# Kernel optimization log

Hardware: AMD Instinct MI355X
Metric: run time of the kernel (lower is better)

## Reference

```python
import jax, jax.numpy as jnp
import numpy as np

N_NODES = 50000


def _gine_conv(x, src, dst, edge_attr, ew, eb, w1, b1, w2, b2, eps=0.0):
    # message: ReLU(x_j + Linear(edge_attr))  -- PyG GINEConv with edge_dim lin
    m = jax.nn.relu(x[src] + edge_attr @ ew + eb)          # [E, D]
    agg = jax.ops.segment_sum(m, dst, num_segments=N_NODES)  # [N, D]
    h = (1.0 + eps) * x + agg
    # nn: Linear -> ReLU -> Linear
    return jax.nn.relu(h @ w1 + b1) @ w2 + b2


def setup_inputs() -> dict:
    key = jax.random.key(0)
    ks = jax.random.split(key, 16)
    Cin, H, Cout, Ed = 128, 256, 256, 16
    E = 800000
    x = jax.random.normal(ks[0], (N_NODES, Cin), dtype=jnp.float32)
    edge_index = jax.random.randint(ks[1], (2, E), 0, N_NODES, dtype=jnp.int32)
    edge_attr = jax.random.normal(ks[2], (E, Ed), dtype=jnp.float32)

    def lin(k, fan_in, fan_out):
        s = 1.0 / np.sqrt(fan_in)
        kw, kb = jax.random.split(k)
        w = jax.random.uniform(kw, (fan_in, fan_out), minval=-s, maxval=s, dtype=jnp.float32)
        b = jax.random.uniform(kb, (fan_out,), minval=-s, maxval=s, dtype=jnp.float32)
        return w, b

    e1_w, e1_b = lin(ks[3], Ed, Cin)     # conv1 edge lin: edge_dim -> in_channels
    l11_w, l11_b = lin(ks[4], Cin, H)    # conv1 MLP layer 1
    l12_w, l12_b = lin(ks[5], H, Cout)   # conv1 MLP layer 2
    e2_w, e2_b = lin(ks[6], Ed, H)       # conv2 edge lin: edge_dim -> hidden
    l21_w, l21_b = lin(ks[7], H, H)      # conv2 MLP layer 1
    l22_w, l22_b = lin(ks[8], H, Cout)   # conv2 MLP layer 2
    return {
        "x": x, "edge_index": edge_index, "edge_attr": edge_attr,
        "e1_w": e1_w, "e1_b": e1_b, "l11_w": l11_w, "l11_b": l11_b,
        "l12_w": l12_w, "l12_b": l12_b,
        "e2_w": e2_w, "e2_b": e2_b, "l21_w": l21_w, "l21_b": l21_b,
        "l22_w": l22_w, "l22_b": l22_b,
    }


def reference(x, edge_index, edge_attr,
              e1_w, e1_b, l11_w, l11_b, l12_w, l12_b,
              e2_w, e2_b, l21_w, l21_b, l22_w, l22_b):
    src, dst = edge_index[0], edge_index[1]
    h = _gine_conv(x, src, dst, edge_attr, e1_w, e1_b, l11_w, l11_b, l12_w, l12_b)
    h = _gine_conv(h, src, dst, edge_attr, e2_w, e2_b, l21_w, l21_b, l22_w, l22_b)
    return h
```

## Files before the change

kernel.cpp:

```cpp
#include <hip/hip_runtime.h>
#include <type_traits>

#define N_NODES 50000

using short8  = __attribute__((ext_vector_type(8))) short;
using floatx4 = __attribute__((ext_vector_type(4))) float;
using f32x2   = __attribute__((ext_vector_type(2))) float;

__device__ inline unsigned short f2b(float f) {
    unsigned u = __float_as_uint(f);
    u += 0x7FFFu + ((u >> 16) & 1u);
    return (unsigned short)(u >> 16);
}
__device__ inline float b2f(unsigned short h) {
    return __uint_as_float(((unsigned)h) << 16);
}

__device__ inline f32x2 pk_fma_lo(f32x2 a, f32x2 b, f32x2 c) {
    f32x2 d;
    asm("v_pk_fma_f32 %0, %1, %2, %3 op_sel_hi:[0,1,1]"
        : "=v"(d) : "v"(a), "v"(b), "v"(c));
    return d;
}
__device__ inline f32x2 pk_fma_hi(f32x2 a, f32x2 b, f32x2 c) {
    f32x2 d;
    asm("v_pk_fma_f32 %0, %1, %2, %3 op_sel:[1,0,0] op_sel_hi:[1,1,1]"
        : "=v"(d) : "v"(a), "v"(b), "v"(c));
    return d;
}
__device__ inline f32x2 pk_add(f32x2 a, f32x2 b) {
    f32x2 d;
    asm("v_pk_add_f32 %0, %1, %2" : "=v"(d) : "v"(a), "v"(b));
    return d;
}

__global__ __launch_bounds__(256) void zero_int_kernel(int* __restrict__ p, int n)
{
    int i = blockIdx.x * 256 + threadIdx.x;
    if (i < n) p[i] = 0;
}

__global__ __launch_bounds__(256) void hist_kernel(const int* __restrict__ dstv,
                                                   int* __restrict__ cnt, int E)
{
    int e = blockIdx.x * 256 + threadIdx.x;
    if (e < E) atomicAdd(&cnt[dstv[e]], 1);
}

__global__ __launch_bounds__(256) void scanA_kernel(const int* __restrict__ cnt,
                                                    int* __restrict__ row_start,
                                                    int* __restrict__ bsum, int n)
{
    __shared__ int s[256];
    int t = threadIdx.x;
    int i = blockIdx.x * 256 + t;
    int val = (i < n) ? cnt[i] : 0;
    s[t] = val;
    __syncthreads();
#pragma unroll
    for (int off = 1; off < 256; off <<= 1) {
        int v = (t >= off) ? s[t - off] : 0;
        __syncthreads();
        s[t] += v;
        __syncthreads();
    }
    if (i < n) row_start[i] = s[t] - val;
    if (t == 255) bsum[blockIdx.x] = s[255];
}

__global__ __launch_bounds__(256) void scanB_kernel(int* __restrict__ bsum, int nb)
{
    __shared__ int s[256];
    int t = threadIdx.x;
    int val = (t < nb) ? bsum[t] : 0;
    s[t] = val;
    __syncthreads();
#pragma unroll
    for (int off = 1; off < 256; off <<= 1) {
        int v = (t >= off) ? s[t - off] : 0;
        __syncthreads();
        s[t] += v;
        __syncthreads();
    }
    if (t < nb) bsum[t] = s[t] - val;
}

__global__ __launch_bounds__(256) void scanC_kernel(int* __restrict__ row_start,
                                                    int* __restrict__ woff,
                                                    const int* __restrict__ bsum, int n)
{
    int i = blockIdx.x * 256 + threadIdx.x;
    if (i < n) {
        int v = row_start[i] + bsum[blockIdx.x];
        row_start[i] = v;
        woff[i] = v;
    }
}

__global__ __launch_bounds__(256) void scatter_kernel(const int* __restrict__ srcv,
                                                      const int* __restrict__ dstv,
                                                      int* __restrict__ woff,
                                                      int2* __restrict__ sorted2, int E)
{
    int e = blockIdx.x * 256 + threadIdx.x;
    if (e < E) {
        int pos = atomicAdd(&woff[dstv[e]], 1);
        sorted2[pos] = make_int2(srcv[e], e);
    }
}

__global__ __launch_bounds__(256) void castT_kernel(const float* __restrict__ w,
                                                    unsigned short* __restrict__ out, int K)
{
    int i = blockIdx.x * 256 + threadIdx.x;
    if (i < K * 256) {
        int k = i >> 8, c = i & 255;
        out[c * K + k] = f2b(w[i]);
    }
}

template<int D, bool XB>
__global__ __launch_bounds__(256) void agg_kernel(
    const float*          __restrict__ xf,
    const unsigned short* __restrict__ xb,
    const float*          __restrict__ ea,
    const float*          __restrict__ ew,
    const float*          __restrict__ ebias,
    const int*            __restrict__ row_start,
    const int*            __restrict__ cnt,
    const int2*           __restrict__ sorted2,
    float*                __restrict__ agg,
    int N)
{
    constexpr int DPL = D / 64;
    constexpr int NP  = DPL / 2;
    using XT = std::conditional_t<XB, ushort4,
               std::conditional_t<DPL == 2, float2, float4>>;

    const int lane = threadIdx.x & 63;
    const int node = blockIdx.x * 4 + (threadIdx.x >> 6);
    if (node >= N) return;
    const int d0 = lane * DPL;

    f32x2 wrp[16 * NP];
#pragma unroll
    for (int k = 0; k < 16; ++k) {
        if constexpr (NP == 1) {
            float2 w2 = *reinterpret_cast<const float2*>(ew + k * D + d0);
            wrp[k] = f32x2{w2.x, w2.y};
        } else {
            float4 w4 = *reinterpret_cast<const float4*>(ew + k * D + d0);
            wrp[k * 2 + 0] = f32x2{w4.x, w4.y};
            wrp[k * 2 + 1] = f32x2{w4.z, w4.w};
        }
    }
    f32x2 bx[NP];
#pragma unroll
    for (int p = 0; p < NP; ++p)
        bx[p] = f32x2{ebias[d0 + p * 2], ebias[d0 + p * 2 + 1]};

    f32x2 acc[NP];
#pragma unroll
    for (int p = 0; p < NP; ++p) acc[p] = f32x2{0.f, 0.f};

    const int s0 = __builtin_amdgcn_readfirstlane(row_start[node]);
    const int c  = __builtin_amdgcn_readfirstlane(cnt[node]);

    for (int base = 0; base < c; base += 64) {
        const int cc = min(64, c - base);

        int2 pr = make_int2(0, 0);
        if (lane < cc) pr = sorted2[s0 + base + lane];

        float4 eA0, eA1, eA2, eA3; XT xA;
        float4 eB0, eB1, eB2, eB3; XT xB;

        auto LOADA = [&](int idx) {
            int s = __builtin_amdgcn_readlane(pr.x, idx);
            int e = __builtin_amdgcn_readlane(pr.y, idx);
            const float4* p = reinterpret_cast<const float4*>(ea + (size_t)e * 16);
            eA0 = p[0]; eA1 = p[1]; eA2 = p[2]; eA3 = p[3];
            if constexpr (XB) xA = *reinterpret_cast<const XT*>(xb + (size_t)s * D + d0);
            else              xA = *reinterpret_cast<const XT*>(xf + (size_t)s * D + d0);
        };
        auto LOADB = [&](int idx) {
            int s = __builtin_amdgcn_readlane(pr.x, idx);
            int e = __builtin_amdgcn_readlane(pr.y, idx);
            const float4* p = reinterpret_cast<const float4*>(ea + (size_t)e * 16);
            eB0 = p[0]; eB1 = p[1]; eB2 = p[2]; eB3 = p[3];
            if constexpr (XB) xB = *reinterpret_cast<const XT*>(xb + (size_t)s * D + d0);
            else              xB = *reinterpret_cast<const XT*>(xf + (size_t)s * D + d0);
        };

        auto COMPUTE = [&](const float4& E0, const float4& E1,
                           const float4& E2, const float4& E3, const XT& X) {
            f32x2 ap[8] = {f32x2{E0.x, E0.y}, f32x2{E0.z, E0.w},
                           f32x2{E1.x, E1.y}, f32x2{E1.z, E1.w},
                           f32x2{E2.x, E2.y}, f32x2{E2.z, E2.w},
                           f32x2{E3.x, E3.y}, f32x2{E3.z, E3.w}};
            f32x2 m[NP];
            if constexpr (XB) {
                m[0] = pk_add(bx[0], f32x2{b2f(X.x), b2f(X.y)});
                m[1] = pk_add(bx[1], f32x2{b2f(X.z), b2f(X.w)});
            } else if constexpr (NP == 1) {
                m[0] = pk_add(bx[0], f32x2{X.x, X.y});
            } else {
                m[0] = pk_add(bx[0], f32x2{X.x, X.y});
                m[1] = pk_add(bx[1], f32x2{X.z, X.w});
            }
#pragma unroll
            for (int kp = 0; kp < 8; ++kp) {
#pragma unroll
                for (int p = 0; p < NP; ++p)
                    m[p] = pk_fma_lo(ap[kp], wrp[(2 * kp) * NP + p], m[p]);
#pragma unroll
                for (int p = 0; p < NP; ++p)
                    m[p] = pk_fma_hi(ap[kp], wrp[(2 * kp + 1) * NP + p], m[p]);
            }
#pragma unroll
            for (int p = 0; p < NP; ++p) {
                f32x2 r{fmaxf(m[p].x, 0.f), fmaxf(m[p].y, 0.f)};
                acc[p] = pk_add(acc[p], r);
            }
        };

        LOADA(0);
        int i = 0;
        while (true) {
            if (i + 1 < cc) LOADB(i + 1);
            COMPUTE(eA0, eA1, eA2, eA3, xA);
            ++i; if (i >= cc) break;
            if (i + 1 < cc) LOADA(i + 1);
            COMPUTE(eB0, eB1, eB2, eB3, xB);
            ++i; if (i >= cc) break;
        }
    }

    if constexpr (NP == 1)
        *reinterpret_cast<float2*>(agg + (size_t)node * D + d0) =
            make_float2(acc[0].x, acc[0].y);
    else
        *reinterpret_cast<float4*>(agg + (size_t)node * D + d0) =
            make_float4(acc[0].x, acc[0].y, acc[1].x, acc[1].y);
}

template<int DIN, bool L1>
__global__ __launch_bounds__(256) void node_mfma_kernel(
    const float*          __restrict__ basef,
    const unsigned short* __restrict__ baseb,
    const float*          __restrict__ agg,
    const unsigned short* __restrict__ w1T,
    const float*          __restrict__ b1,
    const unsigned short* __restrict__ w2T,
    const float*          __restrict__ b2,
    unsigned short*       __restrict__ outb,
    float*                __restrict__ outf,
    int N)
{
    __shared__ unsigned short hs[64 * DIN];
    __shared__ unsigned short ts[64 * 256];
    const int tid = threadIdx.x;
    const int n0 = blockIdx.x * 64;

#pragma unroll
    for (int it = 0; it < (64 * DIN) / (256 * 8); ++it) {
        int flat = (it * 256 + tid) * 8;
        int r = flat / DIN, c = flat % DIN;
        int node = n0 + r;
        float v[8];
        if (node < N) {
            const float* ap = agg + (size_t)node * DIN + c;
            float4 a0 = *reinterpret_cast<const float4*>(ap);
            float4 a1 = *reinterpret_cast<const float4*>(ap + 4);
            float a[8] = {a0.x, a0.y, a0.z, a0.w, a1.x, a1.y, a1.z, a1.w};
            if constexpr (L1) {
                const float* bp = basef + (size_t)node * DIN + c;
                float4 x0 = *reinterpret_cast<const float4*>(bp);
                float4 x1 = *reinterpret_cast<const float4*>(bp + 4);
                float xx[8] = {x0.x, x0.y, x0.z, x0.w, x1.x, x1.y, x1.z, x1.w};
#pragma unroll
                for (int j = 0; j < 8; ++j) v[j] = a[j] + xx[j];
            } else {
                short8 xv = *reinterpret_cast<const short8*>(baseb + (size_t)node * DIN + c);
#pragma unroll
                for (int j = 0; j < 8; ++j) v[j] = a[j] + b2f((unsigned short)xv[j]);
            }
        } else {
#pragma unroll
            for (int j = 0; j < 8; ++j) v[j] = 0.f;
        }
        short8 o;
#pragma unroll
        for (int j = 0; j < 8; ++j) o[j] = (short)f2b(v[j]);
        *reinterpret_cast<short8*>(&hs[r * DIN + (c ^ ((r & 7) << 3))]) = o;
    }
    __syncthreads();

    const int wv = tid >> 6, lane = tid & 63;
    const int lr = lane & 15, lk = (lane >> 4) * 8;
    const int colbase = wv * 64;

    floatx4 acc[4][4];
#pragma unroll
    for (int n = 0; n < 4; ++n) {
        float bn = b1[colbase + n * 16 + lr];
#pragma unroll
        for (int m = 0; m < 4; ++m) acc[m][n] = floatx4{bn, bn, bn, bn};
    }
#pragma unroll
    for (int kk = 0; kk < DIN; kk += 32) {
        short8 af[4], bf[4];
#pragma unroll
        for (int m = 0; m < 4; ++m) {
            int row = m * 16 + lr;
            af[m] = *reinterpret_cast<const short8*>(
                &hs[row * DIN + ((kk + lk) ^ ((row & 7) << 3))]);
        }
#pragma unroll
        for (int n = 0; n < 4; ++n) {
            int col = colbase + n * 16 + lr;
            bf[n] = *reinterpret_cast<const short8*>(w1T + (size_t)col * DIN + kk + lk);
        }
#pragma unroll
        for (int m = 0; m < 4; ++m)
#pragma unroll
            for (int n = 0; n < 4; ++n)
                acc[m][n] = __builtin_amdgcn_mfma_f32_16x16x32_bf16(af[m], bf[n], acc[m][n], 0, 0, 0);
    }
#pragma unroll
    for (int m = 0; m < 4; ++m)
#pragma unroll
        for (int n = 0; n < 4; ++n)
#pragma unroll
            for (int r = 0; r < 4; ++r) {
                int row = m * 16 + (lane >> 4) * 4 + r;
                int col = colbase + n * 16 + lr;
                ts[row * 256 + (col ^ ((row & 7) << 3))] = f2b(fmaxf(acc[m][n][r], 0.f));
            }
    __syncthreads();

    floatx4 acc2[4][4];
#pragma unroll
    for (int n = 0; n < 4; ++n) {
        float bn = b2[colbase + n * 16 + lr];
#pragma unroll
        for (int m = 0; m < 4; ++m) acc2[m][n] = floatx4{bn, bn, bn, bn};
    }
#pragma unroll
    for (int kk = 0; kk < 256; kk += 32) {
        short8 af[4], bf[4];
#pragma unroll
        for (int m = 0; m < 4; ++m) {
            int row = m * 16 + lr;
            af[m] = *reinterpret_cast<const short8*>(
                &ts[row * 256 + ((kk + lk) ^ ((row & 7) << 3))]);
        }
#pragma unroll
        for (int n = 0; n < 4; ++n) {
            int col = colbase + n * 16 + lr;
            bf[n] = *reinterpret_cast<const short8*>(w2T + (size_t)col * 256 + kk + lk);
        }
#pragma unroll
        for (int m = 0; m < 4; ++m)
#pragma unroll
            for (int n = 0; n < 4; ++n)
                acc2[m][n] = __builtin_amdgcn_mfma_f32_16x16x32_bf16(af[m], bf[n], acc2[m][n], 0, 0, 0);
    }
#pragma unroll
    for (int m = 0; m < 4; ++m)
#pragma unroll
        for (int n = 0; n < 4; ++n)
#pragma unroll
            for (int r = 0; r < 4; ++r) {
                int row = m * 16 + (lane >> 4) * 4 + r;
                int node = n0 + row;
                int col = colbase + n * 16 + lr;
                if (node < N) {
                    if constexpr (L1) outb[(size_t)node * 256 + col] = f2b(acc2[m][n][r]);
                    else              outf[(size_t)node * 256 + col] = acc2[m][n][r];
                }
            }
}

extern "C" void kernel_launch(void* const* d_in, const int* in_sizes, int n_in,
                              void* d_out, int out_size, void* d_ws, size_t ws_size,
                              hipStream_t stream)
{
    const float* x    = (const float*)d_in[0];
    const int*   ei   = (const int*)  d_in[1];
    const float* ea   = (const float*)d_in[2];
    const float* e1w  = (const float*)d_in[3];
    const float* e1b  = (const float*)d_in[4];
    const float* w11  = (const float*)d_in[5];
    const float* b11  = (const float*)d_in[6];
    const float* w12  = (const float*)d_in[7];
    const float* b12  = (const float*)d_in[8];
    const float* e2w  = (const float*)d_in[9];
    const float* e2b  = (const float*)d_in[10];
    const float* w21  = (const float*)d_in[11];
    const float* b21  = (const float*)d_in[12];
    const float* w22  = (const float*)d_in[13];
    const float* b22  = (const float*)d_in[14];

    const int E = in_sizes[1] / 2;
    const int N = N_NODES;
    const int* src = ei;
    const int* dst = ei + E;

    char* cur = (char*)d_ws;
    float* aggb = (float*)cur;            cur += (size_t)N * 256 * 4;
    int*   cnt       = (int*)cur;         cur += (size_t)N * 4;
    int*   row_start = (int*)cur;         cur += (size_t)N * 4;
    int*   woff      = (int*)cur;         cur += (size_t)N * 4;
    int*   bsum      = (int*)cur;         cur += 256 * 4;
    int2*  sorted2   = (int2*)cur;        cur += (size_t)E * 8;
    unsigned short* h1b  = (unsigned short*)cur; cur += (size_t)N * 256 * 2;
    unsigned short* w11T = (unsigned short*)cur; cur += 128 * 256 * 2;
    unsigned short* w12T = (unsigned short*)cur; cur += 256 * 256 * 2;
    unsigned short* w21T = (unsigned short*)cur; cur += 256 * 256 * 2;
    unsigned short* w22T = (unsigned short*)cur; cur += 256 * 256 * 2;
    float* outp = (float*)d_out;

    const int nbN = (N + 255) / 256;
    const int nbE = (E + 255) / 256;

    castT_kernel<<<(128 * 256 + 255) / 256, 256, 0, stream>>>(w11, w11T, 128);
    castT_kernel<<<256, 256, 0, stream>>>(w12, w12T, 256);
    castT_kernel<<<256, 256, 0, stream>>>(w21, w21T, 256);
    castT_kernel<<<256, 256, 0, stream>>>(w22, w22T, 256);

    zero_int_kernel<<<nbN, 256, 0, stream>>>(cnt, N);
    hist_kernel<<<nbE, 256, 0, stream>>>(dst, cnt, E);
    scanA_kernel<<<nbN, 256, 0, stream>>>(cnt, row_start, bsum, N);
    scanB_kernel<<<1, 256, 0, stream>>>(bsum, nbN);
    scanC_kernel<<<nbN, 256, 0, stream>>>(row_start, woff, bsum, N);
    scatter_kernel<<<nbE, 256, 0, stream>>>(src, dst, woff, sorted2, E);

    const int nbAgg  = (N + 3) / 4;
    const int nbNode = (N + 63) / 64;

    agg_kernel<128, false><<<nbAgg, 256, 0, stream>>>(
        x, nullptr, ea, e1w, e1b, row_start, cnt, sorted2, aggb, N);
    node_mfma_kernel<128, true><<<nbNode, 256, 0, stream>>>(
        x, nullptr, aggb, w11T, b11, w12T, b12, h1b, nullptr, N);

    agg_kernel<256, true><<<nbAgg, 256, 0, stream>>>(
        nullptr, h1b, ea, e2w, e2b, row_start, cnt, sorted2, aggb, N);
    node_mfma_kernel<256, false><<<nbNode, 256, 0, stream>>>(
        nullptr, h1b, aggb, w21T, b21, w22T, b22, nullptr, outp, N);
}
```

Baseline: 439.8 us.

## Persistent agg kernel staging edge attrs into LDS with async double buffering

Makes the aggregation kernel persistent: each wave walks over nodes with a grid stride. For each node it stages the edge-attribute rows into a per-wave double-buffered LDS area using global_load_lds, and it prefetches the next node's CSR metadata and edge list while computing the current node. Inside the inner loop, edge attributes are now read from LDS instead of through scalar-indexed global loads. The grid size is fixed and occupancy hints are added to launch_bounds. The cost is explicit vmcnt(0) waits, which may serialize the staging, and the fixed grid sizes may underfill or imbalance the GPU.

Result: slower. 476.3 us (+8.3%).

```diff
diff --git a/kernel.cpp b/kernel.cpp
--- a/kernel.cpp
+++ b/kernel.cpp
@@ -120,7 +120,7 @@
 }
 
 template<int D, bool XB>
-__global__ __launch_bounds__(256) void agg_kernel(
+__global__ __launch_bounds__(256, (D == 256) ? 3 : 4) void agg_kernel(
     const float*          __restrict__ xf,
     const unsigned short* __restrict__ xb,
     const float*          __restrict__ ea,
@@ -137,10 +137,14 @@
     using XT = std::conditional_t<XB, ushort4,
                std::conditional_t<DPL == 2, float2, float4>>;
 
+    __shared__ float sEA[4][2][64][16];
+
     const int lane = threadIdx.x & 63;
-    const int node = blockIdx.x * 4 + (threadIdx.x >> 6);
+    const int w    = threadIdx.x >> 6;
+    const int W    = gridDim.x * 4;
+    int node = blockIdx.x * 4 + w;
+    const int d0 = lane * DPL;
     if (node >= N) return;
-    const int d0 = lane * DPL;
 
     f32x2 wrp[16 * NP];
 #pragma unroll
@@ -157,91 +161,140 @@
     f32x2 bx[NP];
 #pragma unroll
     for (int p = 0; p < NP; ++p)
-        bx[p] = f32x2{ebias[d0 + p * 2], ebias[d0 + p * 2 + 1]};
+        bx[p] = f32x2{ebias[d0 + 2 * p], ebias[d0 + 2 * p + 1]};
 
     f32x2 acc[NP];
-#pragma unroll
-    for (int p = 0; p < NP; ++p) acc[p] = f32x2{0.f, 0.f};
-
-    const int s0 = __builtin_amdgcn_readfirstlane(row_start[node]);
-    const int c  = __builtin_amdgcn_readfirstlane(cnt[node]);
-
-    for (int base = 0; base < c; base += 64) {
-        const int cc = min(64, c - base);
-
-        int2 pr = make_int2(0, 0);
-        if (lane < cc) pr = sorted2[s0 + base + lane];
-
-        float4 eA0, eA1, eA2, eA3; XT xA;
-        float4 eB0, eB1, eB2, eB3; XT xB;
-
-        auto LOADA = [&](int idx) {
-            int s = __builtin_amdgcn_readlane(pr.x, idx);
-            int e = __builtin_amdgcn_readlane(pr.y, idx);
-            const float4* p = reinterpret_cast<const float4*>(ea + (size_t)e * 16);
-            eA0 = p[0]; eA1 = p[1]; eA2 = p[2]; eA3 = p[3];
+
+    auto STAGE = [&](int2 prv, int cb, int bi) {
+        const int sweeps = (cb + 15) >> 4;
+        const int chunk  = lane & 3;
+        const int sl0    = lane >> 2;
+        for (int j = 0; j < sweeps; ++j) {
+            int sl  = j * 16 + sl0;
+            int eid = __shfl(prv.y, sl);
+            if (sl >= cb) eid = 0;
+            const float* gp = ea + (size_t)eid * 16 + chunk * 4;
+            __builtin_amdgcn_global_load_lds(gp, &sEA[w][bi][j * 16][0], 16, 0, 0);
+        }
+    };
+
+    auto COMPUTE = [&](const float4& E0, const float4& E1,
+                       const float4& E2, const float4& E3, const XT& X) {
+        f32x2 ap[8] = {f32x2{E0.x, E0.y}, f32x2{E0.z, E0.w},
+                       f32x2{E1.x, E1.y}, f32x2{E1.z, E1.w},
+                       f32x2{E2.x, E2.y}, f32x2{E2.z, E2.w},
+                       f32x2{E3.x, E3.y}, f32x2{E3.z, E3.w}};
+        f32x2 m[NP];
+        if constexpr (XB) {
+            m[0] = pk_add(bx[0], f32x2{b2f(X.x), b2f(X.y)});
+            m[1] = pk_add(bx[1], f32x2{b2f(X.z), b2f(X.w)});
+        } else if constexpr (NP == 1) {
+            m[0] = pk_add(bx[0], f32x2{X.x, X.y});
+        } else {
+            m[0] = pk_add(bx[0], f32x2{X.x, X.y});
+            m[1] = pk_add(bx[1], f32x2{X.z, X.w});
+        }
+#pragma unroll
+        for (int kp = 0; kp < 8; ++kp) {
+#pragma unroll
+            for (int p = 0; p < NP; ++p)
+                m[p] = pk_fma_lo(ap[kp], wrp[(2 * kp) * NP + p], m[p]);
+#pragma unroll
+            for (int p = 0; p < NP; ++p)
+                m[p] = pk_fma_hi(ap[kp], wrp[(2 * kp + 1) * NP + p], m[p]);
+        }
+#pragma unroll
+        for (int p = 0; p < NP; ++p) {
+            f32x2 r{fmaxf(m[p].x, 0.f), fmaxf(m[p].y, 0.f)};
+            acc[p] = pk_add(acc[p], r);
+        }
+    };
+
+    auto RUN = [&](int cb, int bi, int2 prv) {
+        if (cb <= 0) return;
+        float4 EA0, EA1, EA2, EA3, EB0, EB1, EB2, EB3;
+        XT xA, xB;
+        auto LA = [&](int i) {
+            const float4* rp = reinterpret_cast<const float4*>(&sEA[w][bi][i][0]);
+            EA0 = rp[0]; EA1 = rp[1]; EA2 = rp[2]; EA3 = rp[3];
+            int s = __builtin_amdgcn_readlane(prv.x, i);
             if constexpr (XB) xA = *reinterpret_cast<const XT*>(xb + (size_t)s * D + d0);
             else              xA = *reinterpret_cast<const XT*>(xf + (size_t)s * D + d0);
         };
-        auto LOADB = [&](int idx) {
-            int s = __builtin_amdgcn_readlane(pr.x, idx);
-            int e = __builtin_amdgcn_readlane(pr.y, idx);
-            const float4* p = reinterpret_cast<const float4*>(ea + (size_t)e * 16);
-            eB0 = p[0]; eB1 = p[1]; eB2 = p[2]; eB3 = p[3];
+        auto LB = [&](int i) {
+            const float4* rp = reinterpret_cast<const float4*>(&sEA[w][bi][i][0]);
+            EB0 = rp[0]; EB1 = rp[1]; EB2 = rp[2]; EB3 = rp[3];
+            int s = __builtin_amdgcn_readlane(prv.x, i);
             if constexpr (XB) xB = *reinterpret_cast<const XT*>(xb + (size_t)s * D + d0);
             else              xB = *reinterpret_cast<const XT*>(xf + (size_t)s * D + d0);
         };
-
-        auto COMPUTE = [&](const float4& E0, const float4& E1,
-                           const float4& E2, const float4& E3, const XT& X) {
-            f32x2 ap[8] = {f32x2{E0.x, E0.y}, f32x2{E0.z, E0.w},
-                           f32x2{E1.x, E1.y}, f32x2{E1.z, E1.w},
-                           f32x2{E2.x, E2.y}, f32x2{E2.z, E2.w},
-                           f32x2{E3.x, E3.y}, f32x2{E3.z, E3.w}};
-            f32x2 m[NP];
-            if constexpr (XB) {
-                m[0] = pk_add(bx[0], f32x2{b2f(X.x), b2f(X.y)});
-                m[1] = pk_add(bx[1], f32x2{b2f(X.z), b2f(X.w)});
-            } else if constexpr (NP == 1) {
-                m[0] = pk_add(bx[0], f32x2{X.x, X.y});
-            } else {
-                m[0] = pk_add(bx[0], f32x2{X.x, X.y});
-                m[1] = pk_add(bx[1], f32x2{X.z, X.w});
-            }
-#pragma unroll
-            for (int kp = 0; kp < 8; ++kp) {
-#pragma unroll
-                for (int p = 0; p < NP; ++p)
-                    m[p] = pk_fma_lo(ap[kp], wrp[(2 * kp) * NP + p], m[p]);
-#pragma unroll
-                for (int p = 0; p < NP; ++p)
-                    m[p] = pk_fma_hi(ap[kp], wrp[(2 * kp + 1) * NP + p], m[p]);
-            }
-#pragma unroll
-            for (int p = 0; p < NP; ++p) {
-                f32x2 r{fmaxf(m[p].x, 0.f), fmaxf(m[p].y, 0.f)};
-                acc[p] = pk_add(acc[p], r);
-            }
-        };
-
-        LOADA(0);
+        LA(0);
         int i = 0;
         while (true) {
-            if (i + 1 < cc) LOADB(i + 1);
-            COMPUTE(eA0, eA1, eA2, eA3, xA);
-            ++i; if (i >= cc) break;
-            if (i + 1 < cc) LOADA(i + 1);
-            COMPUTE(eB0, eB1, eB2, eB3, xB);
-            ++i; if (i >= cc) break;
-        }
-    }
-
-    if constexpr (NP == 1)
-        *reinterpret_cast<float2*>(agg + (size_t)node * D + d0) =
-            make_float2(acc[0].x, acc[0].y);
-    else
-        *reinterpret_cast<float4*>(agg + (size_t)node * D + d0) =
-            make_float4(acc[0].x, acc[0].y, acc[1].x, acc[1].y);
+            if (i + 1 < cb) LB(i + 1);
+            COMPUTE(EA0, EA1, EA2, EA3, xA);
+            ++i; if (i >= cb) break;
+            if (i + 1 < cb) LA(i + 1);
+            COMPUTE(EB0, EB1, EB2, EB3, xB);
+            ++i; if (i >= cb) break;
+        }
+    };
+
+    int s0 = __builtin_amdgcn_readfirstlane(row_start[node]);
+    int c  = __builtin_amdgcn_readfirstlane(cnt[node]);
+    int cb = min(c, 64);
+    int2 pr = make_int2(0, 0);
+    if (lane < cb) pr = sorted2[s0 + lane];
+    STAGE(pr, cb, 0);
+    int buf = 0;
+
+    int nnode = node + W;
+    int ns0 = 0, nc = 0;
+    if (nnode < N) { ns0 = row_start[nnode]; nc = cnt[nnode]; }
+
+    asm volatile("s_waitcnt vmcnt(0)" ::: "memory");
+
+    while (true) {
+        int  ncb = 0;
+        int2 npr = make_int2(0, 0);
+        if (nnode < N) {
+            ns0 = __builtin_amdgcn_readfirstlane(ns0);
+            nc  = __builtin_amdgcn_readfirstlane(nc);
+            ncb = min(nc, 64);
+            if (lane < ncb) npr = sorted2[ns0 + lane];
+        }
+        int nnnode = nnode + W;
+        int nns0 = 0, nnc = 0;
+        if (nnnode < N) { nns0 = row_start[nnnode]; nnc = cnt[nnnode]; }
+
+#pragma unroll
+        for (int p = 0; p < NP; ++p) acc[p] = f32x2{0.f, 0.f};
+
+        RUN(cb, buf, pr);
+
+        for (int base = 64; base < c; base += 64) {
+            int cb2 = min(64, c - base);
+            int2 pv = make_int2(0, 0);
+            if (lane < cb2) pv = sorted2[s0 + base + lane];
+            STAGE(pv, cb2, buf);
+            asm volatile("s_waitcnt vmcnt(0)" ::: "memory");
+            RUN(cb2, buf, pv);
+        }
+
+        if constexpr (NP == 1)
+            *reinterpret_cast<float2*>(agg + (size_t)node * D + d0) =
+                make_float2(acc[0].x, acc[0].y);
+        else
+            *reinterpret_cast<float4*>(agg + (size_t)node * D + d0) =
+                make_float4(acc[0].x, acc[0].y, acc[1].x, acc[1].y);
+
+        if (nnode >= N) break;
+        STAGE(npr, ncb, buf ^ 1);
+        asm volatile("s_waitcnt vmcnt(0)" ::: "memory");
+
+        node = nnode; s0 = ns0; c = nc; cb = ncb; pr = npr; buf ^= 1;
+        nnode = nnnode; ns0 = nns0; nc = nnc;
+    }
 }
 
 template<int DIN, bool L1>
@@ -436,15 +489,14 @@
     scanC_kernel<<<nbN, 256, 0, stream>>>(row_start, woff, bsum, N);
     scatter_kernel<<<nbE, 256, 0, stream>>>(src, dst, woff, sorted2, E);
 
-    const int nbAgg  = (N + 3) / 4;
     const int nbNode = (N + 63) / 64;
 
-    agg_kernel<128, false><<<nbAgg, 256, 0, stream>>>(
+    agg_kernel<128, false><<<1024, 256, 0, stream>>>(
         x, nullptr, ea, e1w, e1b, row_start, cnt, sorted2, aggb, N);
     node_mfma_kernel<128, true><<<nbNode, 256, 0, stream>>>(
         x, nullptr, aggb, w11T, b11, w12T, b12, h1b, nullptr, N);
 
-    agg_kernel<256, true><<<nbAgg, 256, 0, stream>>>(
+    agg_kernel<256, true><<<768, 256, 0, stream>>>(
         nullptr, h1b, ea, e2w, e2b, row_start, cnt, sorted2, aggb, N);
     node_mfma_kernel<256, false><<<nbNode, 256, 0, stream>>>(
         nullptr, h1b, aggb, w21T, b21, w22T, b22, nullptr, outp, N);
```

## Stage edge-linear weights in LDS and process edges in pairs

Applied to the files above, without the earlier changes.

The aggregation kernel now loads the 16xD edge-linear weights and bias into shared memory once per block and reads them from LDS inside the inner loop, instead of holding them in registers. This frees a large register array, which should allow more waves per CU. The edge loop also changes from a software-pipelined A/B prefetch to processing two edges per iteration so each LDS weight read serves both. The cost is extra LDS traffic on every iteration and the loss of the explicit prefetch overlap between load and compute.

Result: faster. 415.4 us (-5.5%).

```diff
diff --git a/kernel.cpp b/kernel.cpp
--- a/kernel.cpp
+++ b/kernel.cpp
@@ -28,10 +28,8 @@
         : "=v"(d) : "v"(a), "v"(b), "v"(c));
     return d;
 }
-__device__ inline f32x2 pk_add(f32x2 a, f32x2 b) {
-    f32x2 d;
-    asm("v_pk_add_f32 %0, %1, %2" : "=v"(d) : "v"(a), "v"(b));
-    return d;
+__device__ inline f32x2 vrelu(f32x2 a) {
+    return __builtin_elementwise_max(a, f32x2{0.f, 0.f});
 }
 
 __global__ __launch_bounds__(256) void zero_int_kernel(int* __restrict__ p, int n)
@@ -137,27 +135,33 @@
     using XT = std::conditional_t<XB, ushort4,
                std::conditional_t<DPL == 2, float2, float4>>;
 
-    const int lane = threadIdx.x & 63;
-    const int node = blockIdx.x * 4 + (threadIdx.x >> 6);
+    __shared__ float wlds[17 * D];
+
+    const int tid = threadIdx.x;
+#pragma unroll
+    for (int ci = tid; ci < (17 * D) / 4; ci += 256) {
+        int f0 = ci * 4;
+        float4 v;
+        if (f0 < 16 * D) v = *reinterpret_cast<const float4*>(ew + f0);
+        else             v = *reinterpret_cast<const float4*>(ebias + (f0 - 16 * D));
+        *reinterpret_cast<float4*>(&wlds[f0]) = v;
+    }
+    __syncthreads();
+
+    const int lane = tid & 63;
+    const int node = blockIdx.x * 4 + (tid >> 6);
     if (node >= N) return;
     const int d0 = lane * DPL;
 
-    f32x2 wrp[16 * NP];
-#pragma unroll
-    for (int k = 0; k < 16; ++k) {
-        if constexpr (NP == 1) {
-            float2 w2 = *reinterpret_cast<const float2*>(ew + k * D + d0);
-            wrp[k] = f32x2{w2.x, w2.y};
-        } else {
-            float4 w4 = *reinterpret_cast<const float4*>(ew + k * D + d0);
-            wrp[k * 2 + 0] = f32x2{w4.x, w4.y};
-            wrp[k * 2 + 1] = f32x2{w4.z, w4.w};
-        }
-    }
-    f32x2 bx[NP];
-#pragma unroll
-    for (int p = 0; p < NP; ++p)
-        bx[p] = f32x2{ebias[d0 + p * 2], ebias[d0 + p * 2 + 1]};
+    f32x2 bxp[NP];
+    if constexpr (NP == 1) {
+        float2 bb = *reinterpret_cast<const float2*>(&wlds[16 * D + d0]);
+        bxp[0] = f32x2{bb.x, bb.y};
+    } else {
+        float4 bb = *reinterpret_cast<const float4*>(&wlds[16 * D + d0]);
+        bxp[0] = f32x2{bb.x, bb.y};
+        bxp[1] = f32x2{bb.z, bb.w};
+    }
 
     f32x2 acc[NP];
 #pragma unroll
@@ -166,73 +170,111 @@
     const int s0 = __builtin_amdgcn_readfirstlane(row_start[node]);
     const int c  = __builtin_amdgcn_readfirstlane(cnt[node]);
 
+    auto LOADE = [&](int2 prv, int idx, float4* E, XT& X) {
+        int s = __builtin_amdgcn_readlane(prv.x, idx);
+        int e = __builtin_amdgcn_readlane(prv.y, idx);
+        const float4* p = reinterpret_cast<const float4*>(ea + (size_t)e * 16);
+        E[0] = p[0]; E[1] = p[1]; E[2] = p[2]; E[3] = p[3];
+        if constexpr (XB) X = *reinterpret_cast<const XT*>(xb + (size_t)s * D + d0);
+        else              X = *reinterpret_cast<const XT*>(xf + (size_t)s * D + d0);
+    };
+
+    auto PAIRS = [&](const float4* E, f32x2* ap) {
+        ap[0] = f32x2{E[0].x, E[0].y}; ap[1] = f32x2{E[0].z, E[0].w};
+        ap[2] = f32x2{E[1].x, E[1].y}; ap[3] = f32x2{E[1].z, E[1].w};
+        ap[4] = f32x2{E[2].x, E[2].y}; ap[5] = f32x2{E[2].z, E[2].w};
+        ap[6] = f32x2{E[3].x, E[3].y}; ap[7] = f32x2{E[3].z, E[3].w};
+    };
+
+    auto MINIT = [&](const XT& X, f32x2* m) {
+        if constexpr (XB) {
+            m[0] = bxp[0] + f32x2{b2f(X.x), b2f(X.y)};
+            m[1] = bxp[1] + f32x2{b2f(X.z), b2f(X.w)};
+        } else if constexpr (NP == 1) {
+            m[0] = bxp[0] + f32x2{X.x, X.y};
+        } else {
+            m[0] = bxp[0] + f32x2{X.x, X.y};
+            m[1] = bxp[1] + f32x2{X.z, X.w};
+        }
+    };
+
+    auto KLOOP2 = [&](const f32x2* aA, f32x2* mA, const f32x2* aB, f32x2* mB) {
+#pragma unroll
+        for (int k2 = 0; k2 < 8; ++k2) {
+            f32x2 we[NP], wo[NP];
+            if constexpr (NP == 1) {
+                float2 w0 = *reinterpret_cast<const float2*>(&wlds[(2 * k2) * D + d0]);
+                float2 w1 = *reinterpret_cast<const float2*>(&wlds[(2 * k2 + 1) * D + d0]);
+                we[0] = f32x2{w0.x, w0.y};
+                wo[0] = f32x2{w1.x, w1.y};
+            } else {
+                float4 w0 = *reinterpret_cast<const float4*>(&wlds[(2 * k2) * D + d0]);
+                float4 w1 = *reinterpret_cast<const float4*>(&wlds[(2 * k2 + 1) * D + d0]);
+                we[0] = f32x2{w0.x, w0.y}; we[1] = f32x2{w0.z, w0.w};
+                wo[0] = f32x2{w1.x, w1.y}; wo[1] = f32x2{w1.z, w1.w};
+            }
+#pragma unroll
+            for (int p = 0; p < NP; ++p) mA[p] = pk_fma_lo(aA[k2], we[p], mA[p]);
+#pragma unroll
+            for (int p = 0; p < NP; ++p) mA[p] = pk_fma_hi(aA[k2], wo[p], mA[p]);
+#pragma unroll
+            for (int p = 0; p < NP; ++p) mB[p] = pk_fma_lo(aB[k2], we[p], mB[p]);
+#pragma unroll
+            for (int p = 0; p < NP; ++p) mB[p] = pk_fma_hi(aB[k2], wo[p], mB[p]);
+        }
+    };
+
+    auto KLOOP1 = [&](const f32x2* aA, f32x2* mA) {
+#pragma unroll
+        for (int k2 = 0; k2 < 8; ++k2) {
+            f32x2 we[NP], wo[NP];
+            if constexpr (NP == 1) {
+                float2 w0 = *reinterpret_cast<const float2*>(&wlds[(2 * k2) * D + d0]);
+                float2 w1 = *reinterpret_cast<const float2*>(&wlds[(2 * k2 + 1) * D + d0]);
+                we[0] = f32x2{w0.x, w0.y};
+                wo[0] = f32x2{w1.x, w1.y};
+            } else {
+                float4 w0 = *reinterpret_cast<const float4*>(&wlds[(2 * k2) * D + d0]);
+                float4 w1 = *reinterpret_cast<const float4*>(&wlds[(2 * k2 + 1) * D + d0]);
+                we[0] = f32x2{w0.x, w0.y}; we[1] = f32x2{w0.z, w0.w};
+                wo[0] = f32x2{w1.x, w1.y}; wo[1] = f32x2{w1.z, w1.w};
+            }
+#pragma unroll
+            for (int p = 0; p < NP; ++p) mA[p] = pk_fma_lo(aA[k2], we[p], mA[p]);
+#pragma unroll
+            for (int p = 0; p < NP; ++p) mA[p] = pk_fma_hi(aA[k2], wo[p], mA[p]);
+        }
+    };
+
     for (int base = 0; base < c; base += 64) {
         const int cc = min(64, c - base);
 
         int2 pr = make_int2(0, 0);
         if (lane < cc) pr = sorted2[s0 + base + lane];
 
-        float4 eA0, eA1, eA2, eA3; XT xA;
-        float4 eB0, eB1, eB2, eB3; XT xB;
-
-        auto LOADA = [&](int idx) {
-            int s = __builtin_amdgcn_readlane(pr.x, idx);
-            int e = __builtin_amdgcn_readlane(pr.y, idx);
-            const float4* p = reinterpret_cast<const float4*>(ea + (size_t)e * 16);
-            eA0 = p[0]; eA1 = p[1]; eA2 = p[2]; eA3 = p[3];
-            if constexpr (XB) xA = *reinterpret_cast<const XT*>(xb + (size_t)s * D + d0);
-            else              xA = *reinterpret_cast<const XT*>(xf + (size_t)s * D + d0);
-        };
-        auto LOADB = [&](int idx) {
-            int s = __builtin_amdgcn_readlane(pr.x, idx);
-            int e = __builtin_amdgcn_readlane(pr.y, idx);
-            const float4* p = reinterpret_cast<const float4*>(ea + (size_t)e * 16);
-            eB0 = p[0]; eB1 = p[1]; eB2 = p[2]; eB3 = p[3];
-            if constexpr (XB) xB = *reinterpret_cast<const XT*>(xb + (size_t)s * D + d0);
-            else              xB = *reinterpret_cast<const XT*>(xf + (size_t)s * D + d0);
-        };
-
-        auto COMPUTE = [&](const float4& E0, const float4& E1,
-                           const float4& E2, const float4& E3, const XT& X) {
-            f32x2 ap[8] = {f32x2{E0.x, E0.y}, f32x2{E0.z, E0.w},
-                           f32x2{E1.x, E1.y}, f32x2{E1.z, E1.w},
-                           f32x2{E2.x, E2.y}, f32x2{E2.z, E2.w},
-                           f32x2{E3.x, E3.y}, f32x2{E3.z, E3.w}};
-            f32x2 m[NP];
-            if constexpr (XB) {
-                m[0] = pk_add(bx[0], f32x2{b2f(X.x), b2f(X.y)});
-                m[1] = pk_add(bx[1], f32x2{b2f(X.z), b2f(X.w)});
-            } else if constexpr (NP == 1) {
-                m[0] = pk_add(bx[0], f32x2{X.x, X.y});
-            } else {
-                m[0] = pk_add(bx[0], f32x2{X.x, X.y});
-                m[1] = pk_add(bx[1], f32x2{X.z, X.w});
-            }
-#pragma unroll
-            for (int kp = 0; kp < 8; ++kp) {
-#pragma unroll
-                for (int p = 0; p < NP; ++p)
-                    m[p] = pk_fma_lo(ap[kp], wrp[(2 * kp) * NP + p], m[p]);
-#pragma unroll
-                for (int p = 0; p < NP; ++p)
-                    m[p] = pk_fma_hi(ap[kp], wrp[(2 * kp + 1) * NP + p], m[p]);
-            }
-#pragma unroll
-            for (int p = 0; p < NP; ++p) {
-                f32x2 r{fmaxf(m[p].x, 0.f), fmaxf(m[p].y, 0.f)};
-                acc[p] = pk_add(acc[p], r);
-            }
-        };
-
-        LOADA(0);
+        float4 EA[4], EB[4]; XT xA, xB;
+        f32x2 apA[8], apB[8], mA[NP], mB[NP];
+
         int i = 0;
-        while (true) {
-            if (i + 1 < cc) LOADB(i + 1);
-            COMPUTE(eA0, eA1, eA2, eA3, xA);
-            ++i; if (i >= cc) break;
-            if (i + 1 < cc) LOADA(i + 1);
-            COMPUTE(eB0, eB1, eB2, eB3, xB);
-            ++i; if (i >= cc) break;
+        while (i + 1 < cc) {
+            LOADE(pr, i,     EA, xA);
+            LOADE(pr, i + 1, EB, xB);
+            PAIRS(EA, apA); PAIRS(EB, apB);
+            MINIT(xA, mA);  MINIT(xB, mB);
+            KLOOP2(apA, mA, apB, mB);
+#pragma unroll
+            for (int p = 0; p < NP; ++p) acc[p] = acc[p] + vrelu(mA[p]);
+#pragma unroll
+            for (int p = 0; p < NP; ++p) acc[p] = acc[p] + vrelu(mB[p]);
+            i += 2;
+        }
+        if (i < cc) {
+            LOADE(pr, i, EA, xA);
+            PAIRS(EA, apA);
+            MINIT(xA, mA);
+            KLOOP1(apA, mA);
+#pragma unroll
+            for (int p = 0; p < NP; ++p) acc[p] = acc[p] + vrelu(mA[p]);
         }
     }
 
```
